# Kernel tuning notes

Measured on AMD Instinct MI355X. Metric: run time of the kernel, lower is better.

Reference implementation:

```python
import jax, jax.numpy as jnp
import numpy as np

NUM_NODES = 200000
B = 65536          # n_id batch size
E = 131072         # events per direction
D_MEM = 128
D_RAW = 128
D_TIME = 128
T_MAX = 1000000


def setup_inputs() -> dict:
    key = jax.random.key(0)
    ks = jax.random.split(key, 16)
    inp = {
        'memory': jax.random.normal(ks[0], (NUM_NODES, D_MEM), jnp.float32),
        'last_update': jax.random.randint(ks[1], (NUM_NODES,), 0, 1000, jnp.int64),
        'n_id': jnp.arange(B, dtype=jnp.int64),
        'src_s': jax.random.randint(ks[2], (E,), 0, B, jnp.int64),
        'dst_s': jax.random.randint(ks[3], (E,), 0, B, jnp.int64),
        't_s': jax.random.randint(ks[4], (E,), 0, T_MAX, jnp.int64),
        'raw_msg_s': jax.random.normal(ks[5], (E, D_RAW), jnp.float32),
        'src_d': jax.random.randint(ks[6], (E,), 0, B, jnp.int64),
        'dst_d': jax.random.randint(ks[7], (E,), 0, B, jnp.int64),
        't_d': jax.random.randint(ks[8], (E,), 0, T_MAX, jnp.int64),
        'raw_msg_d': jax.random.normal(ks[9], (E, D_RAW), jnp.float32),
        'w_time': jax.random.normal(ks[10], (D_TIME, 1), jnp.float32) * 0.1,
        'b_time': jax.random.normal(ks[11], (D_TIME,), jnp.float32) * 0.1,
        'W_ih': jax.random.normal(ks[12], (3 * D_MEM, 2 * D_MEM + D_RAW + D_TIME), jnp.float32) * 0.05,
        'W_hh': jax.random.normal(ks[13], (3 * D_MEM, D_MEM), jnp.float32) * 0.05,
        'b_ih': jax.random.normal(ks[14], (3 * D_MEM,), jnp.float32) * 0.05,
        'b_hh': jax.random.normal(ks[15], (3 * D_MEM,), jnp.float32) * 0.05,
    }
    return inp


def _time_enc(t_rel, w_time, b_time):
    # Linear(1, time_dim) followed by cos: cos(t * w + b)
    return jnp.cos(t_rel.astype(jnp.float32)[:, None] * w_time[:, 0][None, :] + b_time)


def reference(memory, last_update, n_id, src_s, dst_s, t_s, raw_msg_s,
              src_d, dst_d, t_d, raw_msg_d, w_time, b_time, W_ih, W_hh, b_ih, b_hh):
    nb = n_id.shape[0]
    # assoc: global node id -> local index within n_id
    assoc = jnp.zeros((memory.shape[0],), dtype=jnp.int32).at[n_id].set(
        jnp.arange(nb, dtype=jnp.int32))

    # source-side messages (IdentityMessage = concat)
    t_enc_s = _time_enc(t_s - last_update[src_s], w_time, b_time)
    msg_s = jnp.concatenate([memory[src_s], memory[dst_s], raw_msg_s, t_enc_s], axis=-1)

    # destination-side messages
    t_enc_d = _time_enc(t_d - last_update[dst_d], w_time, b_time)
    msg_d = jnp.concatenate([memory[dst_d], memory[src_d], raw_msg_d, t_enc_d], axis=-1)

    idx = jnp.concatenate([src_s, dst_d], axis=0)       # [2E] global ids
    msg = jnp.concatenate([msg_s, msg_d], axis=0)       # [2E, 512]
    t = jnp.concatenate([t_s, t_d], axis=0)             # [2E]
    loc = assoc[idx]                                     # [2E] local ids

    # LastAggregator: per local node, pick the message with max t (ties -> latest position)
    ne = t.shape[0]
    key = t * ne + jnp.arange(ne, dtype=t.dtype)         # encode (t, position)
    maxkey = jax.ops.segment_max(key, loc, num_segments=nb)
    count = jax.ops.segment_sum(jnp.ones_like(loc), loc, num_segments=nb)
    has = count > 0
    argm = jnp.where(has, maxkey % ne, 0)
    aggr = jnp.where(has[:, None], msg[argm], 0.0)       # [nb, 512]

    # GRUCell(x=aggr, h=memory[n_id])
    h = memory[n_id]
    gi = aggr @ W_ih.T + b_ih
    gh = h @ W_hh.T + b_hh
    gi_r, gi_z, gi_n = jnp.split(gi, 3, axis=-1)
    gh_r, gh_z, gh_n = jnp.split(gh, 3, axis=-1)
    r = jax.nn.sigmoid(gi_r + gh_r)
    z = jax.nn.sigmoid(gi_z + gh_z)
    n = jnp.tanh(gi_n + r * gh_n)
    new_memory = (1.0 - z) * n + z * h

    new_last_update = last_update.at[idx].set(t)[n_id]
    return new_memory, new_last_update
```

## Files before the change

kernel.cpp:

```cpp
#include <hip/hip_runtime.h>
#include <math.h>

#define NUM_NODES 200000
#define NB        65536
#define EV        131072
#define NE        (2*EV)
#define DM        128
#define KDIM      640
#define NO2       512
#define BM        128
#define BK        64
#define THREADS   1024

typedef float f32x4 __attribute__((ext_vector_type(4)));
typedef unsigned long long u64;

__device__ __forceinline__ float fcos_rev(float rev) {
    float r; asm("v_cos_f32 %0, %1" : "=v"(r) : "v"(rev)); return r;
}
__device__ __forceinline__ float fexp2(float x) {
    float r; asm("v_exp_f32 %0, %1" : "=v"(r) : "v"(x)); return r;
}
__device__ __forceinline__ float frcp(float x) {
    float r; asm("v_rcp_f32 %0, %1" : "=v"(r) : "v"(x)); return r;
}
__device__ __forceinline__ float fast_cos(float arg) {
    double rv = (double)arg * 0.15915494309189535;
    rv -= floor(rv);
    return fcos_rev((float)rv);
}
__device__ __forceinline__ float fsigmoid(float x) {
    x = fminf(fmaxf(x, -30.f), 30.f);
    float e = fexp2(-1.44269504088896f * x);
    return frcp(1.f + e);
}
__device__ __forceinline__ float ftanh_(float x) {
    x = fminf(fmaxf(x, -15.f), 15.f);
    float e = fexp2(-2.88539008177793f * x);
    return (1.f - e) * frcp(1.f + e);
}

#if defined(__has_builtin) && __has_builtin(__builtin_amdgcn_cvt_pk_fp8_f32)
__device__ __forceinline__ unsigned pack4_fp8(float f0, float f1, float f2, float f3) {
    int v = __builtin_amdgcn_cvt_pk_fp8_f32(f0, f1, 0, false);
    v = __builtin_amdgcn_cvt_pk_fp8_f32(f2, f3, v, true);
    return (unsigned)v;
}
#else
__device__ __forceinline__ unsigned enc1_fp8(float x) {
    unsigned u = __float_as_uint(x);
    unsigned s = (u >> 24) & 0x80u;
    float a = fabsf(x);
    if (!(a >= 0.001953125f)) return s;
    if (a > 448.f) a = 448.f;
    int e; float mf = frexpf(a, &e);
    int E = e + 6;
    int mant;
    if (E <= 0) {
        mant = (int)(a * 512.f + 0.5f);
        if (mant > 7) return s | 0x08u;
        return s | (unsigned)mant;
    }
    mant = (int)((mf * 2.f - 1.f) * 8.f + 0.5f);
    if (mant == 8) { mant = 0; ++E; }
    if (E > 15) { E = 15; mant = 6; }
    if (E == 15 && mant == 7) mant = 6;
    return s | (unsigned)(E << 3) | (unsigned)mant;
}
__device__ __forceinline__ unsigned pack4_fp8(float f0, float f1, float f2, float f3) {
    return enc1_fp8(f0) | (enc1_fp8(f1) << 8) | (enc1_fp8(f2) << 16) | (enc1_fp8(f3) << 24);
}
#endif

__global__ void event_scan_k(const int* __restrict__ src_s, const int* __restrict__ t_s,
                             const int* __restrict__ dst_d, const int* __restrict__ t_d,
                             u64* __restrict__ keyarr, u64* __restrict__ lukey) {
    int e = blockIdx.x * 256 + threadIdx.x;
    if (e >= NE) return;
    int g, t;
    if (e < EV) { g = src_s[e];      t = t_s[e]; }
    else        { g = dst_d[e - EV]; t = t_d[e - EV]; }
    u64 key = ((u64)(unsigned)t << 18) + (u64)(unsigned)e + 1ull;
    atomicMax(&keyarr[g], key);
    u64 lk = ((u64)(unsigned)(e + 1) << 20) | (u64)(unsigned)t;
    atomicMax(&lukey[g], lk);
}

__global__ void build_w_k(const float* __restrict__ W_ih, const float* __restrict__ W_hh,
                          const float* __restrict__ b_ih, const float* __restrict__ b_hh,
                          unsigned char* __restrict__ wp8, float* __restrict__ bp) {
    int idx = blockIdx.x * 256 + threadIdx.x;
    if (idx >= NO2 * 80) return;
    int p = idx / 80, g = idx - p * 80;
    int d = p >> 2, gate = p & 3;
    float f[8];
    #pragma unroll
    for (int j = 0; j < 8; ++j) {
        int c = g * 8 + j;
        float v = 0.f;
        if (c < 512) {
            int row = (gate == 0) ? d : (gate == 1) ? 128 + d : (gate == 2) ? 256 + d : -1;
            if (row >= 0) v = W_ih[(size_t)row * 512 + c];
        } else {
            int ch = c - 512;
            int row = (gate == 0) ? d : (gate == 1) ? 128 + d : (gate == 3) ? 256 + d : -1;
            if (row >= 0) v = W_hh[(size_t)row * 128 + ch];
        }
        f[j] = v * 16.f;
    }
    unsigned lo = pack4_fp8(f[0], f[1], f[2], f[3]);
    unsigned hi = pack4_fp8(f[4], f[5], f[6], f[7]);
    u64 q = (u64)lo | ((u64)hi << 32);
    *(u64*)(wp8 + (size_t)(g >> 3) * 32768 + (size_t)(g & 7) * 4096 + (size_t)p * 8) = q;
    if (g == 0) {
        float bv = (gate == 0) ? b_ih[d] + b_hh[d]
                 : (gate == 1) ? b_ih[128 + d] + b_hh[128 + d]
                 : (gate == 2) ? b_ih[256 + d] : b_hh[256 + d];
        bp[p] = bv;
    }
}

__global__ __launch_bounds__(THREADS, 4) void gemm_gru_k(
    const float* __restrict__ memory, const int* __restrict__ last_update,
    const int* __restrict__ src_s, const int* __restrict__ dst_s,
    const int* __restrict__ t_s, const float* __restrict__ raw_s,
    const int* __restrict__ src_d, const int* __restrict__ dst_d,
    const int* __restrict__ t_d, const float* __restrict__ raw_d,
    const float* __restrict__ w_time, const float* __restrict__ b_time,
    const unsigned char* __restrict__ wp8, const float* __restrict__ bp,
    const u64* __restrict__ keyarr, const u64* __restrict__ lukey,
    float* __restrict__ out_mem, float* __restrict__ out_lu)
{
    __shared__ __align__(16) char smem[132096];
    unsigned char* sA = (unsigned char*)smem;
    unsigned char* sB = (unsigned char*)(smem + 16384);
    float* sG = (float*)smem;
    float* sW = (float*)(smem + 114688);
    float* sBt= (float*)(smem + 115200);

    const int tid = threadIdx.x;
    const int m0  = blockIdx.x * BM;
    const int ln  = tid & 63, wid = tid >> 6;
    const int wm  = wid >> 3, wn = wid & 7;
    const int l2  = ln >> 4, rl = ln & 15;

    if (tid < DM) { sW[tid] = w_time[tid]; sBt[tid] = b_time[tid]; }

    const int ar = tid >> 3, ac = tid & 7;
    const int m  = m0 + ar;
    const u64 kk = keyarr[m];
    const int rv = (kk != 0ull);
    int a_ = 0, b_ = 0, t_ = 0;
    const float* pR = raw_s;
    if (kk) {
        int e = (int)((kk - 1ull) & (u64)(NE - 1));
        if (e < EV) { a_ = src_s[e]; b_ = dst_s[e]; t_ = t_s[e]; pR = raw_s + (size_t)e * DM; }
        else { int e2 = e - EV; a_ = dst_d[e2]; b_ = src_d[e2]; t_ = t_d[e2]; pR = raw_d + (size_t)e2 * DM; }
    }
    const float rt = rv ? (float)(t_ - last_update[a_]) : 0.f;
    const float* pA = memory + (size_t)a_ * DM;
    const float* pB = memory + (size_t)b_ * DM;
    const float* pH = memory + (size_t)m  * DM;

    float4 pv0, pv1;
    auto PREF_A = [&](int step) {
        int seg = step >> 1;
        if (seg == 3) return;
        const float* base = (seg == 0) ? pA : (seg == 1) ? pB : (seg == 2) ? pR : pH;
        int off = ((step & 1) << 6) + (ac << 3);
        pv0 = *(const float4*)(base + off);
        pv1 = *(const float4*)(base + off + 4);
    };
    auto STAGE_B = [&](int step, int buf) {
        const unsigned char* src = wp8 + (size_t)step * 32768 + (size_t)tid * 16;
        unsigned char* dst = sB + (size_t)buf * 32768 + (size_t)tid * 16;
        __builtin_amdgcn_global_load_lds((const __attribute__((address_space(1))) void*)src,
            (__attribute__((address_space(3))) void*)dst, 16, 0, 0);
        __builtin_amdgcn_global_load_lds((const __attribute__((address_space(1))) void*)(src + 16384),
            (__attribute__((address_space(3))) void*)(dst + 16384), 16, 0, 0);
    };
    auto WRITE_A = [&](int step, int buf) {
        int seg = step >> 1;
        float f0, f1, f2, f3, f4, f5, f6, f7;
        if (seg == 3) {
            int coff = ((step & 1) << 6) + (ac << 3);
            f0 = fast_cos(__fadd_rn(__fmul_rn(rt, sW[coff+0]), sBt[coff+0]));
            f1 = fast_cos(__fadd_rn(__fmul_rn(rt, sW[coff+1]), sBt[coff+1]));
            f2 = fast_cos(__fadd_rn(__fmul_rn(rt, sW[coff+2]), sBt[coff+2]));
            f3 = fast_cos(__fadd_rn(__fmul_rn(rt, sW[coff+3]), sBt[coff+3]));
            f4 = fast_cos(__fadd_rn(__fmul_rn(rt, sW[coff+4]), sBt[coff+4]));
            f5 = fast_cos(__fadd_rn(__fmul_rn(rt, sW[coff+5]), sBt[coff+5]));
            f6 = fast_cos(__fadd_rn(__fmul_rn(rt, sW[coff+6]), sBt[coff+6]));
            f7 = fast_cos(__fadd_rn(__fmul_rn(rt, sW[coff+7]), sBt[coff+7]));
        } else {
            f0 = pv0.x; f1 = pv0.y; f2 = pv0.z; f3 = pv0.w;
            f4 = pv1.x; f5 = pv1.y; f6 = pv1.z; f7 = pv1.w;
        }
        if (seg < 4 && !rv) { f0=f1=f2=f3=f4=f5=f6=f7 = 0.f; }
        unsigned lo = pack4_fp8(f0, f1, f2, f3);
        unsigned hi = pack4_fp8(f4, f5, f6, f7);
        u64 q = (u64)lo | ((u64)hi << 32);
        *(u64*)(sA + buf * 8192 + ac * 1024 + ar * 8) = q;
    };

    f32x4 acc[4][4];
    #pragma unroll
    for (int mf = 0; mf < 4; ++mf)
        #pragma unroll
        for (int nf = 0; nf < 4; ++nf)
            acc[mf][nf] = (f32x4){0.f, 0.f, 0.f, 0.f};

    PREF_A(0);
    WRITE_A(0, 0);
    STAGE_B(0, 0);
    STAGE_B(1, 1);
    PREF_A(1);
    asm volatile("s_waitcnt vmcnt(4) lgkmcnt(0)" ::: "memory");
    __builtin_amdgcn_sched_barrier(0);
    __builtin_amdgcn_s_barrier();

    #pragma unroll
    for (int k = 0; k < 10; ++k) {
        const int av = k & 1, an = av ^ 1;
        const int bv = k % 3;

        const unsigned char* sAc = sA + av * 8192;
        const unsigned char* sBc = sB + bv * 32768;

        long afr0[4], bfr0[4];
        #pragma unroll
        for (int mf = 0; mf < 4; ++mf)
            afr0[mf] = *(const long*)(sAc + l2 * 1024 + (wm * 64 + mf * 16 + rl) * 8);
        #pragma unroll
        for (int nf = 0; nf < 4; ++nf)
            bfr0[nf] = *(const long*)(sBc + l2 * 4096 + (wn * 64 + nf * 16 + rl) * 8);
        __builtin_amdgcn_sched_barrier(0);

        if (k < 9) WRITE_A(k + 1, an);
        __builtin_amdgcn_sched_barrier(0);
        if (k < 8) STAGE_B(k + 2, (k + 2) % 3);
        __builtin_amdgcn_sched_barrier(0);
        if (k < 8 && ((k + 2) >> 1) != 3) PREF_A(k + 2);
        __builtin_amdgcn_sched_barrier(0);

        __builtin_amdgcn_s_setprio(1);
        #pragma unroll
        for (int mf = 0; mf < 4; ++mf)
            #pragma unroll
            for (int nf = 0; nf < 4; ++nf)
                acc[mf][nf] = __builtin_amdgcn_mfma_f32_16x16x32_fp8_fp8(
                    afr0[mf], bfr0[nf], acc[mf][nf], 0, 0, 0);
        __builtin_amdgcn_s_setprio(0);

        long afr1[4], bfr1[4];
        #pragma unroll
        for (int mf = 0; mf < 4; ++mf)
            afr1[mf] = *(const long*)(sAc + (4 + l2) * 1024 + (wm * 64 + mf * 16 + rl) * 8);
        #pragma unroll
        for (int nf = 0; nf < 4; ++nf)
            bfr1[nf] = *(const long*)(sBc + (4 + l2) * 4096 + (wn * 64 + nf * 16 + rl) * 8);
        __builtin_amdgcn_s_setprio(1);
        #pragma unroll
        for (int mf = 0; mf < 4; ++mf)
            #pragma unroll
            for (int nf = 0; nf < 4; ++nf)
                acc[mf][nf] = __builtin_amdgcn_mfma_f32_16x16x32_fp8_fp8(
                    afr1[mf], bfr1[nf], acc[mf][nf], 0, 0, 0);
        __builtin_amdgcn_s_setprio(0);

        if (k < 9) {
            __builtin_amdgcn_sched_barrier(0);
            if (k < 4 || k == 6 || k == 7)
                asm volatile("s_waitcnt vmcnt(4) lgkmcnt(0)" ::: "memory");
            else if (k == 4 || k == 5)
                asm volatile("s_waitcnt vmcnt(2) lgkmcnt(0)" ::: "memory");
            else
                asm volatile("s_waitcnt vmcnt(0) lgkmcnt(0)" ::: "memory");
            __builtin_amdgcn_sched_barrier(0);
            __builtin_amdgcn_s_barrier();
        }
    }

    if (tid < BM) {
        u64 lk = lukey[m0 + tid];
        out_lu[m0 + tid] = lk ? (float)(unsigned)(lk & 0xFFFFFull)
                              : (float)last_update[m0 + tid];
    }
    __syncthreads();

    const float ds = 0.0625f;
    #pragma unroll
    for (int p = 0; p < 2; ++p) {
        if (wm == p) {
            #pragma unroll
            for (int mf = 0; mf < 4; ++mf)
                #pragma unroll
                for (int nf = 0; nf < 4; ++nf)
                    #pragma unroll
                    for (int reg = 0; reg < 4; ++reg) {
                        int row = mf * 16 + l2 * 4 + reg;
                        int col = wn * 64 + nf * 16 + rl;
                        sG[row * 516 + col] = acc[mf][nf][reg] * ds;
                    }
        }
        __syncthreads();
        #pragma unroll
        for (int i = 0; i < 2; ++i) {
            int idx = tid + i * 1024;
            int row = idx >> 5, dq = idx & 31;
            int gm = m0 + p * 64 + row;
            const float* gr = sG + row * 516 + dq * 16;
            f32x4 g0 = *(const f32x4*)(gr + 0);
            f32x4 g1 = *(const f32x4*)(gr + 4);
            f32x4 g2 = *(const f32x4*)(gr + 8);
            f32x4 g3 = *(const f32x4*)(gr + 12);
            f32x4 bb0 = *(const f32x4*)(bp + dq * 16 + 0);
            f32x4 bb1 = *(const f32x4*)(bp + dq * 16 + 4);
            f32x4 bb2 = *(const f32x4*)(bp + dq * 16 + 8);
            f32x4 bb3 = *(const f32x4*)(bp + dq * 16 + 12);
            f32x4 h = *(const f32x4*)(memory + (size_t)gm * DM + dq * 4);
            f32x4 res;
            {
                float rg = fsigmoid(g0.x + bb0.x);
                float zg = fsigmoid(g0.y + bb0.y);
                float ng = ftanh_(g0.z + bb0.z + rg * (g0.w + bb0.w));
                res.x = (1.f - zg) * ng + zg * h.x;
            }
            {
                float rg = fsigmoid(g1.x + bb1.x);
                float zg = fsigmoid(g1.y + bb1.y);
                float ng = ftanh_(g1.z + bb1.z + rg * (g1.w + bb1.w));
                res.y = (1.f - zg) * ng + zg * h.y;
            }
            {
                float rg = fsigmoid(g2.x + bb2.x);
                float zg = fsigmoid(g2.y + bb2.y);
                float ng = ftanh_(g2.z + bb2.z + rg * (g2.w + bb2.w));
                res.z = (1.f - zg) * ng + zg * h.z;
            }
            {
                float rg = fsigmoid(g3.x + bb3.x);
                float zg = fsigmoid(g3.y + bb3.y);
                float ng = ftanh_(g3.z + bb3.z + rg * (g3.w + bb3.w));
                res.w = (1.f - zg) * ng + zg * h.w;
            }
            *(f32x4*)(out_mem + (size_t)gm * DM + dq * 4) = res;
        }
        if (p == 0) __syncthreads();
    }
}

extern "C" void kernel_launch(void* const* d_in, const int* in_sizes, int n_in,
                              void* d_out, int out_size, void* d_ws, size_t ws_size,
                              hipStream_t stream) {
    const float* memory      = (const float*)d_in[0];
    const int*   last_update = (const int*)d_in[1];
    const int*   src_s       = (const int*)d_in[3];
    const int*   dst_s       = (const int*)d_in[4];
    const int*   t_s         = (const int*)d_in[5];
    const float* raw_s       = (const float*)d_in[6];
    const int*   src_d       = (const int*)d_in[7];
    const int*   dst_d       = (const int*)d_in[8];
    const int*   t_d         = (const int*)d_in[9];
    const float* raw_d       = (const float*)d_in[10];
    const float* w_time      = (const float*)d_in[11];
    const float* b_time      = (const float*)d_in[12];
    const float* W_ih        = (const float*)d_in[13];
    const float* W_hh        = (const float*)d_in[14];
    const float* b_ih        = (const float*)d_in[15];
    const float* b_hh        = (const float*)d_in[16];

    char* ws = (char*)d_ws;
    u64* keyarr = (u64*)ws;
    u64* lukey  = (u64*)(ws + 524288);
    unsigned char* wp8 = (unsigned char*)(ws + 1048576);
    float* bp = (float*)(ws + 1376256);

    hipMemsetAsync(d_ws, 0, 1048576, stream);

    event_scan_k<<<NE / 256, 256, 0, stream>>>(src_s, t_s, dst_d, t_d, keyarr, lukey);
    build_w_k<<<(NO2 * 80 + 255) / 256, 256, 0, stream>>>(W_ih, W_hh, b_ih, b_hh, wp8, bp);

    float* out_mem = (float*)d_out;
    float* out_lu  = out_mem + (size_t)NB * DM;
    gemm_gru_k<<<NB / BM, THREADS, 0, stream>>>(memory, last_update,
        src_s, dst_s, t_s, raw_s, src_d, dst_d, t_d, raw_d,
        w_time, b_time, wp8, bp, keyarr, lukey, out_mem, out_lu);
}
```

Measured before the change: 88.53 us.

## Halve GEMM tile to 64 rows, swizzle LDS layout, and fuse prep kernels

The fused gather+GEMM+GRU kernel now uses 64-row blocks with 512 threads and a smaller LDS footprint, aiming for more resident blocks per CU. A/B tiles in LDS get an XOR swizzle so each lane loads a 16-byte pair of fp8 fragments, and the B buffer becomes double-buffered instead of triple. The epilogue runs per wave through a private LDS slice, with no block-wide barriers. The event scan and weight-packing kernels merge into one launch. The risks are shallower prefetch for B and each block re-streaming the full weight matrix for half the rows.

After: 79.29 us. 1.12x faster.

```diff
diff --git a/kernel.cpp b/kernel.cpp
--- a/kernel.cpp
+++ b/kernel.cpp
@@ -1,18 +1,17 @@
 #include <hip/hip_runtime.h>
 #include <math.h>
 
-#define NUM_NODES 200000
 #define NB        65536
 #define EV        131072
 #define NE        (2*EV)
 #define DM        128
-#define KDIM      640
 #define NO2       512
-#define BM        128
-#define BK        64
-#define THREADS   1024
+#define BM        64
+#define THREADS   512
+#define SWZ(r)    ((((r) ^ ((r) >> 2))) & 3)
 
 typedef float f32x4 __attribute__((ext_vector_type(4)));
+typedef long  longx2 __attribute__((ext_vector_type(2)));
 typedef unsigned long long u64;
 
 __device__ __forceinline__ float fcos_rev(float rev) {
@@ -54,8 +53,7 @@
     if (!(a >= 0.001953125f)) return s;
     if (a > 448.f) a = 448.f;
     int e; float mf = frexpf(a, &e);
-    int E = e + 6;
-    int mant;
+    int E = e + 6, mant;
     if (E <= 0) {
         mant = (int)(a * 512.f + 0.5f);
         if (mant > 7) return s | 0x08u;
@@ -72,31 +70,34 @@
 }
 #endif
 
-__global__ void event_scan_k(const int* __restrict__ src_s, const int* __restrict__ t_s,
-                             const int* __restrict__ dst_d, const int* __restrict__ t_d,
-                             u64* __restrict__ keyarr, u64* __restrict__ lukey) {
-    int e = blockIdx.x * 256 + threadIdx.x;
-    if (e >= NE) return;
-    int g, t;
-    if (e < EV) { g = src_s[e];      t = t_s[e]; }
-    else        { g = dst_d[e - EV]; t = t_d[e - EV]; }
-    u64 key = ((u64)(unsigned)t << 18) + (u64)(unsigned)e + 1ull;
-    atomicMax(&keyarr[g], key);
-    u64 lk = ((u64)(unsigned)(e + 1) << 20) | (u64)(unsigned)t;
-    atomicMax(&lukey[g], lk);
-}
-
-__global__ void build_w_k(const float* __restrict__ W_ih, const float* __restrict__ W_hh,
-                          const float* __restrict__ b_ih, const float* __restrict__ b_hh,
-                          unsigned char* __restrict__ wp8, float* __restrict__ bp) {
-    int idx = blockIdx.x * 256 + threadIdx.x;
-    if (idx >= NO2 * 80) return;
-    int p = idx / 80, g = idx - p * 80;
-    int d = p >> 2, gate = p & 3;
+__global__ void prep_k(const int* __restrict__ src_s, const int* __restrict__ t_s,
+                       const int* __restrict__ dst_d, const int* __restrict__ t_d,
+                       u64* __restrict__ keyarr, u64* __restrict__ lukey,
+                       const float* __restrict__ W_ih, const float* __restrict__ W_hh,
+                       const float* __restrict__ b_ih, const float* __restrict__ b_hh,
+                       unsigned char* __restrict__ wp8, float* __restrict__ bp) {
+    int bid = blockIdx.x;
+    if (bid < NE / 256) {
+        int e = bid * 256 + threadIdx.x;
+        int g, t;
+        if (e < EV) { g = src_s[e];      t = t_s[e]; }
+        else        { g = dst_d[e - EV]; t = t_d[e - EV]; }
+        u64 key = ((u64)(unsigned)t << 18) + (u64)(unsigned)e + 1ull;
+        atomicMax(&keyarr[g], key);
+        u64 lk = ((u64)(unsigned)(e + 1) << 20) | (u64)(unsigned)t;
+        atomicMax(&lukey[g], lk);
+        return;
+    }
+    int idx = (bid - NE / 256) * 256 + threadIdx.x;
+    int col = idx / 80, g = idx - col * 80;
+    int step = g >> 3, sl = g & 7;
+    int kg = ((sl >> 1) ^ SWZ(col)) + ((sl & 1) << 2);
+    int k0 = step * 64 + kg * 8;
+    int d = col >> 2, gate = col & 3;
     float f[8];
     #pragma unroll
     for (int j = 0; j < 8; ++j) {
-        int c = g * 8 + j;
+        int c = k0 + j;
         float v = 0.f;
         if (c < 512) {
             int row = (gate == 0) ? d : (gate == 1) ? 128 + d : (gate == 2) ? 256 + d : -1;
@@ -110,13 +111,13 @@
     }
     unsigned lo = pack4_fp8(f[0], f[1], f[2], f[3]);
     unsigned hi = pack4_fp8(f[4], f[5], f[6], f[7]);
-    u64 q = (u64)lo | ((u64)hi << 32);
-    *(u64*)(wp8 + (size_t)(g >> 3) * 32768 + (size_t)(g & 7) * 4096 + (size_t)p * 8) = q;
+    *(u64*)(wp8 + (size_t)step * 32768 + (size_t)col * 64 + (size_t)sl * 8)
+        = (u64)lo | ((u64)hi << 32);
     if (g == 0) {
         float bv = (gate == 0) ? b_ih[d] + b_hh[d]
                  : (gate == 1) ? b_ih[128 + d] + b_hh[128 + d]
                  : (gate == 2) ? b_ih[256 + d] : b_hh[256 + d];
-        bp[p] = bv;
+        bp[col] = bv;
     }
 }
 
@@ -131,17 +132,15 @@
     const u64* __restrict__ keyarr, const u64* __restrict__ lukey,
     float* __restrict__ out_mem, float* __restrict__ out_lu)
 {
-    __shared__ __align__(16) char smem[132096];
+    __shared__ __align__(16) char smem[74752];
     unsigned char* sA = (unsigned char*)smem;
-    unsigned char* sB = (unsigned char*)(smem + 16384);
-    float* sG = (float*)smem;
-    float* sW = (float*)(smem + 114688);
-    float* sBt= (float*)(smem + 115200);
+    unsigned char* sB = (unsigned char*)(smem + 8192);
+    float* sW = (float*)(smem + 73728);
+    float* sBt= (float*)(smem + 74240);
 
     const int tid = threadIdx.x;
     const int m0  = blockIdx.x * BM;
-    const int ln  = tid & 63, wid = tid >> 6;
-    const int wm  = wid >> 3, wn = wid & 7;
+    const int ln  = tid & 63, wn = tid >> 6;
     const int l2  = ln >> 4, rl = ln & 15;
 
     if (tid < DM) { sW[tid] = w_time[tid]; sBt[tid] = b_time[tid]; }
@@ -174,10 +173,11 @@
     auto STAGE_B = [&](int step, int buf) {
         const unsigned char* src = wp8 + (size_t)step * 32768 + (size_t)tid * 16;
         unsigned char* dst = sB + (size_t)buf * 32768 + (size_t)tid * 16;
-        __builtin_amdgcn_global_load_lds((const __attribute__((address_space(1))) void*)src,
-            (__attribute__((address_space(3))) void*)dst, 16, 0, 0);
-        __builtin_amdgcn_global_load_lds((const __attribute__((address_space(1))) void*)(src + 16384),
-            (__attribute__((address_space(3))) void*)(dst + 16384), 16, 0, 0);
+        #pragma unroll
+        for (int i = 0; i < 4; ++i)
+            __builtin_amdgcn_global_load_lds(
+                (const __attribute__((address_space(1))) void*)(src + i * 8192),
+                (__attribute__((address_space(3))) void*)(dst + i * 8192), 16, 0, 0);
     };
     auto WRITE_A = [&](int step, int buf) {
         int seg = step >> 1;
@@ -200,7 +200,7 @@
         unsigned lo = pack4_fp8(f0, f1, f2, f3);
         unsigned hi = pack4_fp8(f4, f5, f6, f7);
         u64 q = (u64)lo | ((u64)hi << 32);
-        *(u64*)(sA + buf * 8192 + ac * 1024 + ar * 8) = q;
+        *(u64*)(sA + buf * 4096 + ar * 64 + (((ac & 3) ^ SWZ(ar)) << 4) + ((ac >> 2) << 3)) = q;
     };
 
     f32x4 acc[4][4];
@@ -213,35 +213,37 @@
     PREF_A(0);
     WRITE_A(0, 0);
     STAGE_B(0, 0);
-    STAGE_B(1, 1);
     PREF_A(1);
-    asm volatile("s_waitcnt vmcnt(4) lgkmcnt(0)" ::: "memory");
+    asm volatile("s_waitcnt vmcnt(2) lgkmcnt(0)" ::: "memory");
     __builtin_amdgcn_sched_barrier(0);
     __builtin_amdgcn_s_barrier();
 
     #pragma unroll
     for (int k = 0; k < 10; ++k) {
-        const int av = k & 1, an = av ^ 1;
-        const int bv = k % 3;
-
-        const unsigned char* sAc = sA + av * 8192;
-        const unsigned char* sBc = sB + bv * 32768;
-
-        long afr0[4], bfr0[4];
-        #pragma unroll
-        for (int mf = 0; mf < 4; ++mf)
-            afr0[mf] = *(const long*)(sAc + l2 * 1024 + (wm * 64 + mf * 16 + rl) * 8);
-        #pragma unroll
-        for (int nf = 0; nf < 4; ++nf)
-            bfr0[nf] = *(const long*)(sBc + l2 * 4096 + (wn * 64 + nf * 16 + rl) * 8);
+        const int cur = k & 1, nxt = cur ^ 1;
+
+        longx2 a2[4], b2[4];
+        #pragma unroll
+        for (int mf = 0; mf < 4; ++mf) {
+            int r = mf * 16 + rl;
+            a2[mf] = *(const longx2*)(sA + cur * 4096 + r * 64 + ((l2 ^ SWZ(r)) << 4));
+        }
+        #pragma unroll
+        for (int nf = 0; nf < 4; ++nf) {
+            int c = wn * 64 + nf * 16 + rl;
+            b2[nf] = *(const longx2*)(sB + cur * 32768 + c * 64 + ((l2 ^ SWZ(c)) << 4));
+        }
         __builtin_amdgcn_sched_barrier(0);
 
-        if (k < 9) WRITE_A(k + 1, an);
-        __builtin_amdgcn_sched_barrier(0);
-        if (k < 8) STAGE_B(k + 2, (k + 2) % 3);
-        __builtin_amdgcn_sched_barrier(0);
-        if (k < 8 && ((k + 2) >> 1) != 3) PREF_A(k + 2);
-        __builtin_amdgcn_sched_barrier(0);
+        const bool pf = (k < 8) && (((k + 2) >> 1) != 3);
+        if (k < 9) {
+            WRITE_A(k + 1, nxt);
+            __builtin_amdgcn_sched_barrier(0);
+            STAGE_B(k + 1, nxt);
+            __builtin_amdgcn_sched_barrier(0);
+            if (pf) PREF_A(k + 2);
+            __builtin_amdgcn_sched_barrier(0);
+        }
 
         __builtin_amdgcn_s_setprio(1);
         #pragma unroll
@@ -249,33 +251,19 @@
             #pragma unroll
             for (int nf = 0; nf < 4; ++nf)
                 acc[mf][nf] = __builtin_amdgcn_mfma_f32_16x16x32_fp8_fp8(
-                    afr0[mf], bfr0[nf], acc[mf][nf], 0, 0, 0);
-        __builtin_amdgcn_s_setprio(0);
-
-        long afr1[4], bfr1[4];
-        #pragma unroll
-        for (int mf = 0; mf < 4; ++mf)
-            afr1[mf] = *(const long*)(sAc + (4 + l2) * 1024 + (wm * 64 + mf * 16 + rl) * 8);
-        #pragma unroll
-        for (int nf = 0; nf < 4; ++nf)
-            bfr1[nf] = *(const long*)(sBc + (4 + l2) * 4096 + (wn * 64 + nf * 16 + rl) * 8);
-        __builtin_amdgcn_s_setprio(1);
+                    a2[mf].x, b2[nf].x, acc[mf][nf], 0, 0, 0);
         #pragma unroll
         for (int mf = 0; mf < 4; ++mf)
             #pragma unroll
             for (int nf = 0; nf < 4; ++nf)
                 acc[mf][nf] = __builtin_amdgcn_mfma_f32_16x16x32_fp8_fp8(
-                    afr1[mf], bfr1[nf], acc[mf][nf], 0, 0, 0);
+                    a2[mf].y, b2[nf].y, acc[mf][nf], 0, 0, 0);
         __builtin_amdgcn_s_setprio(0);
 
         if (k < 9) {
             __builtin_amdgcn_sched_barrier(0);
-            if (k < 4 || k == 6 || k == 7)
-                asm volatile("s_waitcnt vmcnt(4) lgkmcnt(0)" ::: "memory");
-            else if (k == 4 || k == 5)
-                asm volatile("s_waitcnt vmcnt(2) lgkmcnt(0)" ::: "memory");
-            else
-                asm volatile("s_waitcnt vmcnt(0) lgkmcnt(0)" ::: "memory");
+            if (pf) asm volatile("s_waitcnt vmcnt(2) lgkmcnt(0)" ::: "memory");
+            else    asm volatile("s_waitcnt vmcnt(0) lgkmcnt(0)" ::: "memory");
             __builtin_amdgcn_sched_barrier(0);
             __builtin_amdgcn_s_barrier();
         }
@@ -288,65 +276,58 @@
     }
     __syncthreads();
 
+    float* ep = (float*)(smem + wn * 4352);
+    const int row16 = ln >> 2, dgrp = ln & 3;
+    const int dbase = wn * 16 + dgrp * 4;
     const float ds = 0.0625f;
+    f32x4 bb0 = *(const f32x4*)(bp + (dbase + 0) * 4);
+    f32x4 bb1 = *(const f32x4*)(bp + (dbase + 1) * 4);
+    f32x4 bb2 = *(const f32x4*)(bp + (dbase + 2) * 4);
+    f32x4 bb3 = *(const f32x4*)(bp + (dbase + 3) * 4);
+
     #pragma unroll
-    for (int p = 0; p < 2; ++p) {
-        if (wm == p) {
+    for (int mf = 0; mf < 4; ++mf) {
+        #pragma unroll
+        for (int nf = 0; nf < 4; ++nf)
             #pragma unroll
-            for (int mf = 0; mf < 4; ++mf)
-                #pragma unroll
-                for (int nf = 0; nf < 4; ++nf)
-                    #pragma unroll
-                    for (int reg = 0; reg < 4; ++reg) {
-                        int row = mf * 16 + l2 * 4 + reg;
-                        int col = wn * 64 + nf * 16 + rl;
-                        sG[row * 516 + col] = acc[mf][nf][reg] * ds;
-                    }
-        }
-        __syncthreads();
-        #pragma unroll
-        for (int i = 0; i < 2; ++i) {
-            int idx = tid + i * 1024;
-            int row = idx >> 5, dq = idx & 31;
-            int gm = m0 + p * 64 + row;
-            const float* gr = sG + row * 516 + dq * 16;
-            f32x4 g0 = *(const f32x4*)(gr + 0);
-            f32x4 g1 = *(const f32x4*)(gr + 4);
-            f32x4 g2 = *(const f32x4*)(gr + 8);
-            f32x4 g3 = *(const f32x4*)(gr + 12);
-            f32x4 bb0 = *(const f32x4*)(bp + dq * 16 + 0);
-            f32x4 bb1 = *(const f32x4*)(bp + dq * 16 + 4);
-            f32x4 bb2 = *(const f32x4*)(bp + dq * 16 + 8);
-            f32x4 bb3 = *(const f32x4*)(bp + dq * 16 + 12);
-            f32x4 h = *(const f32x4*)(memory + (size_t)gm * DM + dq * 4);
-            f32x4 res;
-            {
-                float rg = fsigmoid(g0.x + bb0.x);
-                float zg = fsigmoid(g0.y + bb0.y);
-                float ng = ftanh_(g0.z + bb0.z + rg * (g0.w + bb0.w));
-                res.x = (1.f - zg) * ng + zg * h.x;
-            }
-            {
-                float rg = fsigmoid(g1.x + bb1.x);
-                float zg = fsigmoid(g1.y + bb1.y);
-                float ng = ftanh_(g1.z + bb1.z + rg * (g1.w + bb1.w));
-                res.y = (1.f - zg) * ng + zg * h.y;
-            }
-            {
-                float rg = fsigmoid(g2.x + bb2.x);
-                float zg = fsigmoid(g2.y + bb2.y);
-                float ng = ftanh_(g2.z + bb2.z + rg * (g2.w + bb2.w));
-                res.z = (1.f - zg) * ng + zg * h.z;
-            }
-            {
-                float rg = fsigmoid(g3.x + bb3.x);
-                float zg = fsigmoid(g3.y + bb3.y);
-                float ng = ftanh_(g3.z + bb3.z + rg * (g3.w + bb3.w));
-                res.w = (1.f - zg) * ng + zg * h.w;
-            }
-            *(f32x4*)(out_mem + (size_t)gm * DM + dq * 4) = res;
-        }
-        if (p == 0) __syncthreads();
+            for (int j = 0; j < 4; ++j)
+                ep[((ln >> 4) * 4 + j) * 68 + nf * 16 + rl] = acc[mf][nf][j] * ds;
+        asm volatile("s_waitcnt lgkmcnt(0)" ::: "memory");
+
+        const int gm = m0 + mf * 16 + row16;
+        const float* gr = ep + row16 * 68 + dgrp * 16;
+        f32x4 g0 = *(const f32x4*)(gr + 0);
+        f32x4 g1 = *(const f32x4*)(gr + 4);
+        f32x4 g2 = *(const f32x4*)(gr + 8);
+        f32x4 g3 = *(const f32x4*)(gr + 12);
+        f32x4 h  = *(const f32x4*)(memory + (size_t)gm * DM + dbase);
+        f32x4 res;
+        {
+            float rg = fsigmoid(g0.x + bb0.x);
+            float zg = fsigmoid(g0.y + bb0.y);
+            float ng = ftanh_(g0.z + bb0.z + rg * (g0.w + bb0.w));
+            res.x = (1.f - zg) * ng + zg * h.x;
+        }
+        {
+            float rg = fsigmoid(g1.x + bb1.x);
+            float zg = fsigmoid(g1.y + bb1.y);
+            float ng = ftanh_(g1.z + bb1.z + rg * (g1.w + bb1.w));
+            res.y = (1.f - zg) * ng + zg * h.y;
+        }
+        {
+            float rg = fsigmoid(g2.x + bb2.x);
+            float zg = fsigmoid(g2.y + bb2.y);
+            float ng = ftanh_(g2.z + bb2.z + rg * (g2.w + bb2.w));
+            res.z = (1.f - zg) * ng + zg * h.z;
+        }
+        {
+            float rg = fsigmoid(g3.x + bb3.x);
+            float zg = fsigmoid(g3.y + bb3.y);
+            float ng = ftanh_(g3.z + bb3.z + rg * (g3.w + bb3.w));
+            res.w = (1.f - zg) * ng + zg * h.w;
+        }
+        *(f32x4*)(out_mem + (size_t)gm * DM + dbase) = res;
+        if (mf < 3) asm volatile("s_waitcnt lgkmcnt(0)" ::: "memory");
     }
 }
 
@@ -378,8 +359,8 @@
 
     hipMemsetAsync(d_ws, 0, 1048576, stream);
 
-    event_scan_k<<<NE / 256, 256, 0, stream>>>(src_s, t_s, dst_d, t_d, keyarr, lukey);
-    build_w_k<<<(NO2 * 80 + 255) / 256, 256, 0, stream>>>(W_ih, W_hh, b_ih, b_hh, wp8, bp);
+    prep_k<<<NE / 256 + (NO2 * 80) / 256, 256, 0, stream>>>(
+        src_s, t_s, dst_d, t_d, keyarr, lukey, W_ih, W_hh, b_ih, b_hh, wp8, bp);
 
     float* out_mem = (float*)d_out;
     float* out_lu  = out_mem + (size_t)NB * DM;
```
